# Performance work log

Measured on AMD Instinct MI355X. Metric: run time of the kernel, lower is better.

Reference implementation:

```python
import jax, jax.numpy as jnp
import numpy as np

N, T = 4096, 128
D, R = 8, 32
ENC_H, NADE_H, K_MIX = 64, 64, 10


def setup_inputs() -> dict:
    key = jax.random.key(0)
    ks = jax.random.split(key, 17)
    s = 0.1
    rn = lambda k, shp, sc: (sc * jax.random.normal(k, shp)).astype(jnp.float32)
    return {
        "x": rn(ks[0], (N, 1, T), 1.0),
        "enc1_w": rn(ks[1], (1, ENC_H), s),
        "enc1_b": rn(ks[2], (ENC_H,), s),
        "enc2_w": rn(ks[3], (ENC_H, D), s),
        "enc2_b": rn(ks[4], (D,), s),
        "A": rn(ks[5], (R, D, R), s),
        "init_w": rn(ks[6], (1, R), s),
        "nade1_w": rn(ks[7], (R, NADE_H), s),
        "nade1_b": rn(ks[8], (NADE_H,), s),
        "nade2_w": rn(ks[9], (NADE_H, NADE_H), s),
        "nade2_b": rn(ks[10], (NADE_H,), s),
        "mu_w": rn(ks[11], (NADE_H, K_MIX), s),
        "mu_b": rn(ks[12], (K_MIX,), s),
        "sig_w": rn(ks[13], (NADE_H, K_MIX), s),
        "sig_b": rn(ks[14], (K_MIX,), s),
        "alpha_w": rn(ks[15], (NADE_H, K_MIX), s),
        "alpha_b": rn(ks[16], (K_MIX,), s),
    }


def reference(x, enc1_w, enc1_b, enc2_w, enc2_b, A, init_w,
              nade1_w, nade1_b, nade2_w, nade2_b,
              mu_w, mu_b, sig_w, sig_b, alpha_w, alpha_b):
    LOG2PI = jnp.log(2.0 * jnp.pi).astype(x.dtype)

    def phi(x_t, h):
        # x_t: [N], h: [N, R] -> mixture-of-Gaussians log prob [N]
        h = jnp.tanh(h)
        h = jax.nn.relu(h @ nade1_w + nade1_b)
        h = jax.nn.relu(h @ nade2_w + nade2_b)
        mu = h @ mu_w + mu_b                       # [N, K]
        log_sig = h @ sig_w + sig_b                # sig = exp(log_sig)
        log_alpha = jax.nn.log_softmax(h @ alpha_w + alpha_b, axis=1)
        z = (x_t[:, None] - mu) * jnp.exp(-log_sig)
        comp_lp = -0.5 * z * z - log_sig - 0.5 * LOG2PI
        return jax.scipy.special.logsumexp(log_alpha + comp_lp, axis=1)

    xt = x[:, 0, :]                                # [N, T]
    # vectorized encoder over all timesteps: tanh(relu(x*W1+b1)@W2+b2) -> [N, T, D]
    e = jax.nn.relu(xt[:, :, None] * enc1_w[0] + enc1_b)
    enc = jnp.tanh(e @ enc2_w + enc2_b)

    h0 = jnp.broadcast_to(init_w, (xt.shape[0], R))
    res0 = phi(xt[:, 0], h0)

    def step(carry, inputs):
        tmp, res = carry
        e_prev, x_cur = inputs                     # [N, D], [N]
        tmp = jnp.einsum('nd,ni,idj->nj', e_prev, tmp, A)
        res = res + phi(x_cur, tmp)
        return (tmp, res), None

    xs = (jnp.moveaxis(enc[:, :-1, :], 1, 0),      # [T-1, N, D]
          jnp.moveaxis(xt[:, 1:], 1, 0))           # [T-1, N]
    (_, res), _ = jax.lax.scan(step, (h0, res0), xs)
    return jnp.exp(res)
```

## Files before the change

### kernel.cpp

```cpp
#include <hip/hip_runtime.h>

#define DEV __device__ __forceinline__

typedef __attribute__((ext_vector_type(8))) short short8v;
typedef __attribute__((ext_vector_type(4))) float f32x4;

DEV unsigned short bfr(float f) {
    unsigned u = __float_as_uint(f);
    return (unsigned short)((u + 0x7fffu + ((u >> 16) & 1u)) >> 16);
}
DEV short bft(float f) { return (short)(__float_as_uint(f) >> 16); }
DEV float bf2f(unsigned short h) { return __uint_as_float(((unsigned)h) << 16); }
DEV float frcp(float x) { return __builtin_amdgcn_rcpf(x); }
DEV float ftanh(float x) { float e = __expf(2.0f * x); return 1.0f - 2.0f * frcp(e + 1.0f); }

constexpr int NN = 4096, TT = 128, RING = 32;
#define MFMA32(a, b, c) __builtin_amdgcn_mfma_f32_16x16x32_bf16(a, b, c, 0, 0, 0)


__global__ __launch_bounds__(512) __attribute__((amdgpu_waves_per_eu(2)))
void wfa_kernel(
    const float* __restrict__ x,
    const float* __restrict__ e1w, const float* __restrict__ e1b,
    const float* __restrict__ e2w, const float* __restrict__ e2b,
    const float* __restrict__ A,
    const float* __restrict__ initw,
    const float* __restrict__ n1w, const float* __restrict__ n1b,
    const float* __restrict__ n2w, const float* __restrict__ n2b,
    const float* __restrict__ muw, const float* __restrict__ mub,
    const float* __restrict__ sgw, const float* __restrict__ sgb,
    const float* __restrict__ alw, const float* __restrict__ alb,
    float* __restrict__ out)
{
    __shared__ __align__(16) unsigned short enc_l[TT * 128];
    __shared__ __align__(16) float x_l[16 * 130];
    __shared__ __align__(16) short8v ring_l[RING][64];
    __shared__ __align__(16) float n1b_l[64], n2b_l[64], hb_l[48];
    __shared__ float part_l[8][16];
    __shared__ int head_l;
    __shared__ int ticket_l;
    __shared__ int prog_l[7];

    const int tid = threadIdx.x;
    const int wv = tid >> 6, lane = tid & 63;
    const int quad = lane >> 4, col = lane & 15;
    const int n0 = blockIdx.x * 16;
    const f32x4 z4 = {0.f, 0.f, 0.f, 0.f};

    for (int i = tid; i < 16 * TT; i += 512)
        x_l[(i >> 7) * 130 + (i & 127)] = x[(n0 + (i >> 7)) * TT + (i & 127)];
    if (tid < 64) { n1b_l[tid] = n1b[tid]; n2b_l[tid] = n2b[tid]; }
    if (tid >= 64 && tid < 112) {
        const int i = tid - 64, mt = i >> 4, k = i & 15;
        hb_l[i] = (k < 10) ? ((mt == 0) ? mub[k] : (mt == 1) ? sgb[k] : alb[k]) : 0.f;
    }
    if (tid >= 112 && tid < 119) prog_l[tid - 112] = (tid == 115) ? (1 << 30) : 0;
    if (tid == 120) { head_l = 0; ticket_l = 0; }

    __syncthreads();

    {
        float e1c[16], e1bc[16];
        #pragma unroll
        for (int kc = 0; kc < 2; ++kc)
            #pragma unroll
            for (int jj = 0; jj < 8; ++jj) {
                const int f = kc * 32 + (jj >> 2) * 16 + quad * 4 + (jj & 3);
                e1c[kc * 8 + jj] = e1w[f];
                e1bc[kc * 8 + jj] = e1b[f];
            }
        short8v E2A[2];
        #pragma unroll
        for (int kc = 0; kc < 2; ++kc)
            #pragma unroll
            for (int jj = 0; jj < 8; ++jj)
                E2A[kc][jj] = (short)(col < 8
                    ? bfr(e2w[(kc * 32 + (jj >> 2) * 16 + quad * 4 + (jj & 3)) * 8 + col]) : 0);
        float e2bc[4];
        #pragma unroll
        for (int r = 0; r < 4; ++r) e2bc[r] = (quad < 2) ? e2b[quad * 4 + r] : 0.f;

        const int tbase = wv * 16;
        #pragma unroll 1
        for (int nn = 0; nn < 16; ++nn) {
            const float xs = x_l[nn * 130 + tbase + col];
            short8v eB[2];
            #pragma unroll
            for (int kc = 0; kc < 2; ++kc)
                #pragma unroll
                for (int jj = 0; jj < 8; ++jj)
                    eB[kc][jj] = bft(fmaxf(fmaf(xs, e1c[kc * 8 + jj], e1bc[kc * 8 + jj]), 0.f));
            f32x4 d = MFMA32(E2A[0], eB[0], z4);
            d = MFMA32(E2A[1], eB[1], d);
            if (quad < 2) {
                #pragma unroll
                for (int r = 0; r < 4; ++r)
                    enc_l[(tbase + col) * 128 + nn * 8 + quad * 4 + r] = bfr(ftanh(d[r] + e2bc[r]));
            }
        }
    }
    __syncthreads();

    if (wv == 0) {
        short8v A2f[16];
        #pragma unroll
        for (int mt = 0; mt < 16; ++mt)
            #pragma unroll
            for (int jj = 0; jj < 8; ++jj)
                A2f[mt][jj] = (short)bfr(
                    A[((jj >> 2) * 16 + quad * 4 + (jj & 3)) * 256 + (mt >> 1) * 32 + (mt & 1) * 16 + col]);

        short8v tmpB;
        #pragma unroll
        for (int jj = 0; jj < 8; ++jj)
            tmpB[jj] = (short)bfr(initw[(jj >> 2) * 16 + quad * 4 + (jj & 3)]);

        asm volatile("s_setprio 2");

        short8v e8c = *(const short8v*)&enc_l[0 * 128 + col * 8];

        #pragma unroll 1
        for (int t = 0; t < TT; ++t) {
            if (t > 0) {
                const short8v e8n = *(const short8v*)&enc_l[t * 128 + col * 8];
                float ev[8];
                #pragma unroll
                for (int d = 0; d < 8; ++d) ev[d] = bf2f((unsigned short)e8c[d]);
                f32x4 D[16];
                #pragma unroll
                for (int m = 0; m < 16; ++m) D[m] = MFMA32(A2f[m], tmpB, z4);
                short8v nt;
                #pragma unroll
                for (int h = 0; h < 2; ++h)
                    #pragma unroll
                    for (int r = 0; r < 4; ++r) {
                        float sa = ev[0] * D[h][r];
                        float sb = ev[4] * D[8 + h][r];
                        #pragma unroll
                        for (int d = 1; d < 4; ++d) {
                            sa = fmaf(ev[d],     D[2 * d + h][r],     sa);
                            sb = fmaf(ev[d + 4], D[2 * d + 8 + h][r], sb);
                        }
                        nt[h * 4 + r] = bft(sa + sb);
                    }
                __builtin_amdgcn_sched_group_barrier(0x100, 1, 0);
                __builtin_amdgcn_sched_group_barrier(0x008, 16, 0);
                __builtin_amdgcn_sched_group_barrier(0x002, 120, 0);
                tmpB = nt;
                e8c = e8n;
            }
            ring_l[t & (RING - 1)][lane] = tmpB;
            if ((t & 3) == 3) {
                __threadfence_block();
                if (lane == 0) *(volatile int*)&head_l = t + 1;
            }
            if ((t & 7) == 7 && t >= RING - 1 && t < 120) {
                const int need = t + 9 - RING;
                while (true) {
                    int p = (lane < 7) ? *(volatile int*)&prog_l[lane] : (1 << 30);
                    #pragma unroll
                    for (int s = 1; s < 64; s <<= 1) {
                        const int q = __shfl_xor(p, s, 64);
                        p = (q < p) ? q : p;
                    }
                    if (p >= need) break;
                    __builtin_amdgcn_s_sleep(4);
                }
            }
        }
        if (lane < 16) part_l[0][lane] = 0.f;
    } else if (wv == 4) {
        if (lane < 16) part_l[4][lane] = 0.f;
    } else {
        short8v W1f[4];
        #pragma unroll
        for (int mt = 0; mt < 4; ++mt)
            #pragma unroll
            for (int jj = 0; jj < 8; ++jj)
                W1f[mt][jj] = (short)bfr(n1w[((jj >> 2) * 16 + quad * 4 + (jj & 3)) * 64 + mt * 16 + col]);
        short8v W2f[4][2];
        #pragma unroll
        for (int mt = 0; mt < 4; ++mt)
            #pragma unroll
            for (int kb = 0; kb < 2; ++kb)
                #pragma unroll
                for (int jj = 0; jj < 8; ++jj)
                    W2f[mt][kb][jj] = (short)bfr(
                        n2w[(kb * 32 + (jj >> 2) * 16 + quad * 4 + (jj & 3)) * 64 + mt * 16 + col]);
        short8v Whf[3][2];
        #pragma unroll
        for (int mt = 0; mt < 3; ++mt) {
            const float* Wh = (mt == 0) ? muw : (mt == 1) ? sgw : alw;
            #pragma unroll
            for (int kb = 0; kb < 2; ++kb)
                #pragma unroll
                for (int jj = 0; jj < 8; ++jj)
                    Whf[mt][kb][jj] = (short)(col < 10
                        ? bfr(Wh[(kb * 32 + (jj >> 2) * 16 + quad * 4 + (jj & 3)) * 10 + col]) : 0);
        }

        float res2 = 0.f;
        const float CST = 0.91893853320467274f;
        const int c = wv - 1;

        int t;
        if (lane == 0) { t = atomicAdd(&ticket_l, 1); *(volatile int*)&prog_l[c] = t; }
        t = __shfl(t, 0, 64);

        while (t < TT) {
            while (__hip_atomic_load(&head_l, __ATOMIC_ACQUIRE,
                                     __HIP_MEMORY_SCOPE_WORKGROUP) <= t)
                __builtin_amdgcn_s_sleep(1);
            const short8v tf = ring_l[t & (RING - 1)][lane];
            __threadfence_block();
            int tn;
            if (lane == 0) { tn = atomicAdd(&ticket_l, 1); *(volatile int*)&prog_l[c] = tn; }
            tn = __shfl(tn, 0, 64);

            short8v thB;
            #pragma unroll
            for (int jj = 0; jj < 8; ++jj)
                thB[jj] = bft(ftanh(bf2f((unsigned short)tf[jj])));

            short8v h1B[2];
            #pragma unroll
            for (int mt = 0; mt < 4; ++mt) {
                const f32x4 cc = *(const f32x4*)&n1b_l[mt * 16 + quad * 4];
                const f32x4 d = MFMA32(W1f[mt], thB, cc);
                #pragma unroll
                for (int r = 0; r < 4; ++r)
                    h1B[mt >> 1][(mt & 1) * 4 + r] = bft(fmaxf(d[r], 0.f));
            }
            short8v h2B[2];
            #pragma unroll
            for (int mt = 0; mt < 4; ++mt) {
                const f32x4 cc = *(const f32x4*)&n2b_l[mt * 16 + quad * 4];
                f32x4 d = MFMA32(W2f[mt][0], h1B[0], cc);
                d = MFMA32(W2f[mt][1], h1B[1], d);
                #pragma unroll
                for (int r = 0; r < 4; ++r)
                    h2B[mt >> 1][(mt & 1) * 4 + r] = bft(fmaxf(d[r], 0.f));
            }
            f32x4 hd[3];
            #pragma unroll
            for (int mt = 0; mt < 3; ++mt) {
                const f32x4 cc = *(const f32x4*)&hb_l[mt * 16 + quad * 4];
                f32x4 d = MFMA32(Whf[mt][0], h2B[0], cc);
                hd[mt] = MFMA32(Whf[mt][1], h2B[1], d);
            }
            const float xt = x_l[col * 130 + t];
            float s1 = 0.f, s2 = 0.f;
            #pragma unroll
            for (int r = 0; r < 4; ++r) {
                const bool valid = (quad * 4 + r) < 10;
                const float mu = hd[0][r], sg = hd[1][r], la = hd[2][r];
                const float e1t = __expf(la);
                const float z = (xt - mu) * __expf(-sg);
                const float e2t = __expf(la - sg - fmaf(0.5f * z, z, CST));
                s1 += valid ? e1t : 0.f;
                s2 += valid ? e2t : 0.f;
            }
            s1 += __shfl_xor(s1, 16, 64);  s2 += __shfl_xor(s2, 16, 64);
            s1 += __shfl_xor(s1, 32, 64);  s2 += __shfl_xor(s2, 32, 64);
            res2 += __log2f(s2) - __log2f(s1);

            t = tn;
        }
        if (lane == 0) *(volatile int*)&prog_l[c] = 1 << 30;
        if (lane < 16) part_l[wv][lane] = res2;
    }

    __syncthreads();
    if (tid < 16) {
        float s = 0.f;
        #pragma unroll
        for (int w = 0; w < 8; ++w) s += part_l[w][tid];
        out[n0 + tid] = exp2f(s);
    }
}

extern "C" void kernel_launch(void* const* d_in, const int* in_sizes, int n_in,
                              void* d_out, int out_size, void* d_ws, size_t ws_size,
                              hipStream_t stream) {
    wfa_kernel<<<dim3(NN / 16), dim3(512), 0, stream>>>(
        (const float*)d_in[0],  (const float*)d_in[1],  (const float*)d_in[2],
        (const float*)d_in[3],  (const float*)d_in[4],  (const float*)d_in[5],
        (const float*)d_in[6],  (const float*)d_in[7],  (const float*)d_in[8],
        (const float*)d_in[9],  (const float*)d_in[10], (const float*)d_in[11],
        (const float*)d_in[12], (const float*)d_in[13], (const float*)d_in[14],
        (const float*)d_in[15], (const float*)d_in[16], (float*)d_out);
}
```

Baseline: 141.7 us.

## Fold encoder weights into MFMA operand and accumulate recurrence in MFMA chain

The recurrence step used to run 16 independent MFMAs on the bf16 state and then contract the outputs with the encoder vector through about 120 scalar FMAs. It now pre-scales the fp32 state by each encoder component, packs the products to bf16 and accumulates all contributions inside four chained MFMA accumulators. This removes most of the VALU contraction from the serial critical path, but makes the MFMAs dependent chains instead of independent issues. A 8 KB shared padding array is also added, which appears meant to limit occupancy or placement, and state values are now truncated at a different point, which changes rounding.

```diff
diff --git a/kernel.cpp b/kernel.cpp
--- a/kernel.cpp
+++ b/kernel.cpp
@@ -4,6 +4,7 @@
 
 typedef __attribute__((ext_vector_type(8))) short short8v;
 typedef __attribute__((ext_vector_type(4))) float f32x4;
+typedef __attribute__((ext_vector_type(4))) int int4v;
 
 DEV unsigned short bfr(float f) {
     unsigned u = __float_as_uint(f);
@@ -13,6 +14,10 @@
 DEV float bf2f(unsigned short h) { return __uint_as_float(((unsigned)h) << 16); }
 DEV float frcp(float x) { return __builtin_amdgcn_rcpf(x); }
 DEV float ftanh(float x) { float e = __expf(2.0f * x); return 1.0f - 2.0f * frcp(e + 1.0f); }
+
+DEV int pk2(float a, float b) {
+    return (int)__builtin_amdgcn_perm(__float_as_uint(a), __float_as_uint(b), 0x07060302u);
+}
 
 constexpr int NN = 4096, TT = 128, RING = 32;
 #define MFMA32(a, b, c) __builtin_amdgcn_mfma_f32_16x16x32_bf16(a, b, c, 0, 0, 0)
@@ -37,6 +42,7 @@
     __shared__ __align__(16) short8v ring_l[RING][64];
     __shared__ __align__(16) float n1b_l[64], n2b_l[64], hb_l[48];
     __shared__ float part_l[8][16];
+    __shared__ float pad_l[2048];
     __shared__ int head_l;
     __shared__ int ticket_l;
     __shared__ int prog_l[7];
@@ -56,6 +62,7 @@
     }
     if (tid >= 112 && tid < 119) prog_l[tid - 112] = (tid == 115) ? (1 << 30) : 0;
     if (tid == 120) { head_l = 0; ticket_l = 0; }
+    if (tid == 121) ((volatile float*)pad_l)[0] = 0.f;
 
     __syncthreads();
 
@@ -110,10 +117,10 @@
                 A2f[mt][jj] = (short)bfr(
                     A[((jj >> 2) * 16 + quad * 4 + (jj & 3)) * 256 + (mt >> 1) * 32 + (mt & 1) * 16 + col]);
 
-        short8v tmpB;
+        float tmpf[8];
         #pragma unroll
         for (int jj = 0; jj < 8; ++jj)
-            tmpB[jj] = (short)bfr(initw[(jj >> 2) * 16 + quad * 4 + (jj & 3)]);
+            tmpf[jj] = initw[(jj >> 2) * 16 + quad * 4 + (jj & 3)];
 
         asm volatile("s_setprio 2");
 
@@ -126,30 +133,51 @@
                 float ev[8];
                 #pragma unroll
                 for (int d = 0; d < 8; ++d) ev[d] = bf2f((unsigned short)e8c[d]);
-                f32x4 D[16];
-                #pragma unroll
-                for (int m = 0; m < 16; ++m) D[m] = MFMA32(A2f[m], tmpB, z4);
-                short8v nt;
-                #pragma unroll
-                for (int h = 0; h < 2; ++h)
+
+                int4v u0, u4;
+                #pragma unroll
+                for (int k = 0; k < 4; ++k) {
+                    u0[k] = pk2(ev[0] * tmpf[2 * k + 1], ev[0] * tmpf[2 * k]);
+                    u4[k] = pk2(ev[4] * tmpf[2 * k + 1], ev[4] * tmpf[2 * k]);
+                }
+                f32x4 aA0 = MFMA32(A2f[0], *(const short8v*)&u0, z4);
+                f32x4 aA1 = MFMA32(A2f[1], *(const short8v*)&u0, z4);
+                f32x4 aB0 = MFMA32(A2f[8], *(const short8v*)&u4, z4);
+                f32x4 aB1 = MFMA32(A2f[9], *(const short8v*)&u4, z4);
+                #pragma unroll
+                for (int d = 1; d < 4; ++d) {
+                    int4v ud, ue;
                     #pragma unroll
-                    for (int r = 0; r < 4; ++r) {
-                        float sa = ev[0] * D[h][r];
-                        float sb = ev[4] * D[8 + h][r];
-                        #pragma unroll
-                        for (int d = 1; d < 4; ++d) {
-                            sa = fmaf(ev[d],     D[2 * d + h][r],     sa);
-                            sb = fmaf(ev[d + 4], D[2 * d + 8 + h][r], sb);
-                        }
-                        nt[h * 4 + r] = bft(sa + sb);
+                    for (int k = 0; k < 4; ++k) {
+                        ud[k] = pk2(ev[d]     * tmpf[2 * k + 1], ev[d]     * tmpf[2 * k]);
+                        ue[k] = pk2(ev[d + 4] * tmpf[2 * k + 1], ev[d + 4] * tmpf[2 * k]);
                     }
+                    aA0 = MFMA32(A2f[2 * d],     *(const short8v*)&ud, aA0);
+                    aA1 = MFMA32(A2f[2 * d + 1], *(const short8v*)&ud, aA1);
+                    aB0 = MFMA32(A2f[2 * d + 8], *(const short8v*)&ue, aB0);
+                    aB1 = MFMA32(A2f[2 * d + 9], *(const short8v*)&ue, aB1);
+                }
+                #pragma unroll
+                for (int r = 0; r < 4; ++r) {
+                    tmpf[r]     = aA0[r] + aB0[r];
+                    tmpf[4 + r] = aA1[r] + aB1[r];
+                }
                 __builtin_amdgcn_sched_group_barrier(0x100, 1, 0);
-                __builtin_amdgcn_sched_group_barrier(0x008, 16, 0);
-                __builtin_amdgcn_sched_group_barrier(0x002, 120, 0);
-                tmpB = nt;
+                __builtin_amdgcn_sched_group_barrier(0x002, 34, 0);
+                __builtin_amdgcn_sched_group_barrier(0x008, 4, 0);
+                __builtin_amdgcn_sched_group_barrier(0x002, 24, 0);
+                __builtin_amdgcn_sched_group_barrier(0x008, 4, 0);
+                __builtin_amdgcn_sched_group_barrier(0x002, 24, 0);
+                __builtin_amdgcn_sched_group_barrier(0x008, 4, 0);
+                __builtin_amdgcn_sched_group_barrier(0x002, 24, 0);
+                __builtin_amdgcn_sched_group_barrier(0x008, 4, 0);
                 e8c = e8n;
             }
-            ring_l[t & (RING - 1)][lane] = tmpB;
+            int4v rp;
+            #pragma unroll
+            for (int k = 0; k < 4; ++k)
+                rp[k] = pk2(tmpf[2 * k + 1], tmpf[2 * k]);
+            ring_l[t & (RING - 1)][lane] = *(const short8v*)&rp;
             if ((t & 3) == 3) {
                 __threadfence_block();
                 if (lane == 0) *(volatile int*)&head_l = t + 1;
```

Measured after the change: 157.9 us. 1.11x slower.
